# Optimization experiments

Measured on AMD Instinct MI355X. Metric: run time of the kernel, lower is better.

The kernel has to match this reference:

```python
import jax, jax.numpy as jnp
import numpy as np

N_ITERS = 100   # fixed ADMM (OSQP-style) iteration count
RHO = 1.0       # ADMM penalty
SIGMA = 1e-6    # OSQP regularization


def setup_inputs() -> dict:
    key = jax.random.key(0)
    ks = jax.random.split(key, 12)
    B, S, H, nA = 16384, 512, 1024, 24
    mEq, mIneq = 4, 8
    state = jax.random.normal(ks[0], (B, S), dtype=jnp.float32)
    Aeq = jax.random.normal(ks[1], (mEq, nA), dtype=jnp.float32)
    beq = jax.random.normal(ks[2], (mEq,), dtype=jnp.float32)
    A = jax.random.normal(ks[3], (mIneq, nA), dtype=jnp.float32)
    b = jax.random.uniform(ks[4], (mIneq,), dtype=jnp.float32)
    ub = jnp.ones((nA,), dtype=jnp.float32)
    lb = jnp.zeros((nA,), dtype=jnp.float32)
    # MLP parameters (3 Dense layers as in the flax module)
    W1 = jax.random.normal(ks[5], (S, H), dtype=jnp.float32) / np.sqrt(S).astype(np.float32)
    b1 = jnp.zeros((H,), dtype=jnp.float32)
    W2 = jax.random.normal(ks[6], (H, H), dtype=jnp.float32) / np.sqrt(H).astype(np.float32)
    b2 = jnp.zeros((H,), dtype=jnp.float32)
    W3 = jax.random.normal(ks[7], (H, nA), dtype=jnp.float32) / np.sqrt(H).astype(np.float32)
    b3 = jnp.zeros((nA,), dtype=jnp.float32)
    return dict(state=state, Aeq=Aeq, beq=beq, A=A, b=b, ub=ub, lb=lb,
                W1=W1, b1=b1, W2=W2, b2=b2, W3=W3, b3=b3)


def reference(state, Aeq, beq, A, b, ub, lb, W1, b1, W2, b2, W3, b3):
    # ---- 3-layer MLP ----
    h = jax.nn.relu(state @ W1 + b1)
    h = jax.nn.relu(h @ W2 + b2)
    raw = h @ W3 + b3                      # [B, n]
    n = raw.shape[-1]
    I = jnp.eye(n, dtype=raw.dtype)
    # ---- stack constraints exactly as solve_qp: [Aeq; A_ineq; I; -I] ----
    A_tot = jnp.concatenate([Aeq, A, I, -I], axis=0)            # [M, n]
    neg_inf = jnp.full((A.shape[0],), -jnp.inf, dtype=raw.dtype)
    l_tot = jnp.concatenate([beq, neg_inf, lb, -ub])            # [M]
    u_tot = jnp.concatenate([beq, b, ub, -lb])                  # [M]
    # ---- OSQP-style ADMM: min 0.5||x||^2 - raw'x  s.t. l <= A_tot x <= u ----
    q = -raw                                                    # [B, n]
    M = (1.0 + SIGMA) * I + RHO * (A_tot.T @ A_tot)             # [n, n] (P = I)
    Minv = jnp.linalg.inv(M)
    B_, m = q.shape[0], A_tot.shape[0]
    X0 = jnp.zeros_like(q)
    Z0 = jnp.zeros((B_, m), dtype=q.dtype)
    Y0 = jnp.zeros((B_, m), dtype=q.dtype)

    def step(carry, _):
        X, Z, Y = carry
        rhs = SIGMA * X - q + (RHO * Z - Y) @ A_tot             # [B, n]
        Xn = rhs @ Minv.T                                       # [B, n]
        Zt = Xn @ A_tot.T                                       # [B, m]
        Zn = jnp.clip(Zt + Y / RHO, l_tot, u_tot)
        Yn = Y + RHO * (Zt - Zn)
        return (Xn, Zn, Yn), None

    (X, Z, Y), _ = jax.lax.scan(step, (X0, Z0, Y0), None, length=N_ITERS)
    return X
```

## Files before the change

### kernel.cpp

```cpp
#include <hip/hip_runtime.h>

using uint = unsigned int;
using ushort = unsigned short;

typedef __attribute__((ext_vector_type(8))) short bf16x8;
typedef __attribute__((ext_vector_type(4))) short bf16x4;
typedef __attribute__((ext_vector_type(4))) float f32x4;

#define ADMM_ITERS 100
#define RHO_C 1.0f
#define SIGMA_C 1e-6f

__device__ inline ushort f2bf(float f) {
  union { float f; uint u; } c; c.f = f;
  uint u = c.u;
  uint r = (u + 0x7fffu + ((u >> 16) & 1u)) >> 16;
  return (ushort)r;
}

__device__ inline void gload_lds16(const void* g, void* l) {
  __builtin_amdgcn_global_load_lds(
      (const __attribute__((address_space(1))) void*)g,
      (__attribute__((address_space(3))) void*)l, 16, 0, 0);
}

__device__ inline void splitPack(const float* x, bf16x8& hi, bf16x8& lo) {
#pragma unroll
  for (int j = 0; j < 8; ++j) {
    uint b = __float_as_uint(x[j]);
    uint hb = b & 0xffff0000u;
    float lf = x[j] - __uint_as_float(hb);
    hi[j] = (short)(b >> 16);
    lo[j] = (short)(__float_as_uint(lf) >> 16);
  }
}

__device__ inline void packPairs(const f32x4& x, uint& h0, uint& h1,
                                 uint& l0, uint& l1) {
  uint b0 = __float_as_uint(x[0]), b1 = __float_as_uint(x[1]);
  uint b2 = __float_as_uint(x[2]), b3 = __float_as_uint(x[3]);
  float r0 = x[0] - __uint_as_float(b0 & 0xffff0000u);
  float r1 = x[1] - __uint_as_float(b1 & 0xffff0000u);
  float r2 = x[2] - __uint_as_float(b2 & 0xffff0000u);
  float r3 = x[3] - __uint_as_float(b3 & 0xffff0000u);
  h0 = __builtin_amdgcn_perm(b1, b0, 0x07060302u);
  h1 = __builtin_amdgcn_perm(b3, b2, 0x07060302u);
  l0 = __builtin_amdgcn_perm(__float_as_uint(r1), __float_as_uint(r0), 0x07060302u);
  l1 = __builtin_amdgcn_perm(__float_as_uint(r3), __float_as_uint(r2), 0x07060302u);
}

__device__ inline int permrow(int n) {
  if (n < 32) {
    int j = n & 7;
    return ((j >> 2) << 4) + ((n >> 3) << 2) + (j & 3);
  }
  return n;
}

__device__ void transpose_body(const float* __restrict__ in, ushort* __restrict__ out,
                               int R, int C, int Cout, int bx, int by, int tid) {
  __shared__ float t[32][33];
  const int c0 = bx * 32, r0 = by * 32;
  const int tx = tid & 31, ty = tid >> 5;
  for (int rr = ty; rr < 32; rr += 8) {
    int r = r0 + rr, c = c0 + tx;
    float v = 0.0f;
    if (r < R && c < C) v = in[(long)r * C + c];
    t[rr][tx] = v;
  }
  __syncthreads();
  for (int rr = ty; rr < 32; rr += 8) {
    int c = c0 + rr, r = r0 + tx;
    if (c < Cout && r < R) out[(long)c * R + r] = f2bf(t[tx][rr]);
  }
}

__device__ void setup_body(const float* __restrict__ Aeq, const float* __restrict__ beq,
                           const float* __restrict__ A, const float* __restrict__ b,
                           const float* __restrict__ ub, const float* __restrict__ lb,
                           ushort* __restrict__ Th, ushort* __restrict__ Tl,
                           ushort* __restrict__ T0h, ushort* __restrict__ T0l,
                           float* __restrict__ blp, float* __restrict__ bup, int t) {
  __shared__ float Aug[24][48];
  __shared__ float A12[12 * 24];
  __shared__ float fac[24];
  __shared__ float Tx[24][36];
  for (int i = t; i < 48 * 64; i += 256) { Th[i] = 0; Tl[i] = 0; }
  for (int i = t; i < 48 * 32; i += 256) { T0h[i] = 0; T0l[i] = 0; }
  if (t < 96)  A12[t] = Aeq[t];
  if (t < 192) A12[96 + t] = A[t];
  __syncthreads();
  for (int idx = t; idx < 576; idx += 256) {
    int j = idx / 24, k = idx % 24;
    float s = (j == k) ? (1.0f + SIGMA_C + 2.0f * RHO_C) : 0.0f;
    for (int r = 0; r < 12; ++r) s += RHO_C * A12[r * 24 + j] * A12[r * 24 + k];
    Aug[j][k] = s;
    Aug[j][24 + k] = (j == k) ? 1.0f : 0.0f;
  }
  __syncthreads();
  for (int p = 0; p < 24; ++p) {
    float rp = 1.0f / Aug[p][p];
    if (t < 24) fac[t] = Aug[t][p];
    __syncthreads();
    if (t < 48) Aug[p][t] *= rp;
    __syncthreads();
    for (int idx = t; idx < 24 * 48; idx += 256) {
      int r = idx / 48, c = idx % 48;
      if (r != p) Aug[r][c] -= fac[r] * Aug[p][c];
    }
    __syncthreads();
  }
  auto splitStore = [](ushort* hp, ushort* lp, int i, float v) {
    ushort hs = f2bf(v);
    float hf = __uint_as_float(((uint)hs) << 16);
    ushort ls = f2bf(v - hf);
    hp[i] = hs; lp[i] = ls;
  };
  for (int idx = t; idx < 24 * 36; idx += 256) {
    int n = idx / 36, k = idx % 36;
    float v;
    if (k < 24) v = 2.0f * Aug[n][24 + k];
    else {
      v = 0.0f;
      for (int j = 0; j < 24; ++j) v += Aug[n][24 + j] * A12[(k - 24) * 24 + j];
    }
    Tx[n][k] = v;
    splitStore(Th, Tl, permrow(n) * 64 + k, v);
  }
  __syncthreads();
  for (int idx = t; idx < 12 * 36; idx += 256) {
    int m = idx / 36, k = idx % 36;
    float v = 0.0f;
    for (int j = 0; j < 24; ++j) v += A12[m * 24 + j] * Tx[j][k];
    splitStore(Th, Tl, permrow(24 + m) * 64 + k, v);
  }
  for (int idx = t; idx < 36 * 24; idx += 256) {
    int n = idx / 24, k = idx % 24;
    float v;
    if (n < 24) v = Aug[n][24 + k];
    else {
      v = 0.0f;
      for (int j = 0; j < 24; ++j) v += A12[(n - 24) * 24 + j] * Aug[j][24 + k];
    }
    splitStore(T0h, T0l, permrow(n) * 32 + k, v);
  }
  if (t < 48) {
    float lv, uv;
    if (t < 24)      { lv = lb[t]; uv = ub[t]; }
    else if (t < 28) { lv = beq[t - 24]; uv = lv; }
    else if (t < 36) { lv = -1e30f; uv = b[t - 28]; }
    else             { lv = -1e30f; uv = 1e30f; }
    blp[t] = lv; bup[t] = uv;
  }
}

__global__ void prep_all(
    const float* __restrict__ state, ushort* __restrict__ stateB, int n4,
    const float* __restrict__ W1, ushort* __restrict__ W1T,
    const float* __restrict__ W2, ushort* __restrict__ W2T,
    const float* __restrict__ W3, ushort* __restrict__ W3T,
    const float* __restrict__ Aeq, const float* __restrict__ beq,
    const float* __restrict__ A, const float* __restrict__ b,
    const float* __restrict__ ub, const float* __restrict__ lb,
    ushort* __restrict__ Th, ushort* __restrict__ Tl,
    ushort* __restrict__ T0h, ushort* __restrict__ T0l,
    float* __restrict__ blp, float* __restrict__ bup) {
  const int nConv = n4 >> 8;
  int bb = blockIdx.x;
  if (bb < nConv) {
    int i = bb * 256 + threadIdx.x;
    if (i < n4) {
      float4 v = ((const float4*)state)[i];
      uint2 p;
      p.x = (uint)f2bf(v.x) | ((uint)f2bf(v.y) << 16);
      p.y = (uint)f2bf(v.z) | ((uint)f2bf(v.w) << 16);
      ((uint2*)stateB)[i] = p;
    }
    return;
  }
  bb -= nConv;
  if (bb < 512)  { transpose_body(W1, W1T, 512, 1024, 1024, bb & 31, bb >> 5, threadIdx.x); return; }
  bb -= 512;
  if (bb < 1024) { transpose_body(W2, W2T, 1024, 1024, 1024, bb & 31, bb >> 5, threadIdx.x); return; }
  bb -= 1024;
  if (bb < 32)   { transpose_body(W3, W3T, 1024, 24, 32, 0, bb, threadIdx.x); return; }
  setup_body(Aeq, beq, A, b, ub, lb, Th, Tl, T0h, T0l, blp, bup, threadIdx.x);
}

template<int BM, int BN, int WM, int WN, int TM, int TN, int MODE>
__global__ __launch_bounds__(256) void gemm_bt(
    const ushort* __restrict__ A, const ushort* __restrict__ Bt,
    const float* __restrict__ bias, void* __restrict__ Cout_,
    int K, int ldc, int nvalid) {
  __shared__ char lds[(BM + BN) * 64];
  char* ldsA = lds;
  char* ldsB = lds + BM * 64;

  const int tid = threadIdx.x;
  const int wave = tid >> 6;
  const int lane = tid & 63;
  const int blockM = blockIdx.y * BM;
  const int blockN = blockIdx.x * BN;
  const int wm = (wave / WN) * (TM * 16);
  const int wn = (wave % WN) * (TN * 16);

  f32x4 acc[TM][TN] = {};

  const int l15 = lane & 15;
  const int kq = lane >> 4;
  constexpr int AI = BM / 16;
  constexpr int TOT = (BM + BN) / 16;
  const int srow = lane >> 2;
  const int kb = (lane & 3) ^ ((srow >> 1) & 3);

  for (int k0 = 0; k0 < K; k0 += 32) {
    for (int inst = wave; inst < TOT; inst += 4) {
      const bool isA = inst < AI;
      const int i = isA ? inst : inst - AI;
      const ushort* gp = (isA ? A : Bt)
          + (long)((isA ? blockM : blockN) + i * 16 + srow) * K + (k0 + kb * 8);
      char* lp = (isA ? ldsA : ldsB) + i * 1024;
      gload_lds16(gp, lp);
    }
    __syncthreads();

    bf16x8 af[TM], bfr[TN];
#pragma unroll
    for (int i = 0; i < TM; ++i) {
      int r = wm + i * 16 + l15;
      int ch = kq ^ ((r >> 1) & 3);
      af[i] = *(const bf16x8*)(ldsA + r * 64 + ch * 16);
    }
#pragma unroll
    for (int j = 0; j < TN; ++j) {
      int r = wn + j * 16 + l15;
      int ch = kq ^ ((r >> 1) & 3);
      bfr[j] = *(const bf16x8*)(ldsB + r * 64 + ch * 16);
    }
#pragma unroll
    for (int i = 0; i < TM; ++i)
#pragma unroll
      for (int j = 0; j < TN; ++j)
        acc[i][j] = __builtin_amdgcn_mfma_f32_16x16x32_bf16(af[i], bfr[j], acc[i][j], 0, 0, 0);
    __syncthreads();
  }

  const int ro = lane >> 4;
#pragma unroll
  for (int i = 0; i < TM; ++i) {
#pragma unroll
    for (int j = 0; j < TN; ++j) {
      const int col = blockN + wn + j * 16 + l15;
      float bv;
      if (MODE == 0) bv = bias[col];
      else bv = (col < nvalid) ? bias[col] : 0.0f;
#pragma unroll
      for (int r = 0; r < 4; ++r) {
        const int row = blockM + wm + i * 16 + ro * 4 + r;
        float v = acc[i][j][r] + bv;
        if (MODE == 0) {
          v = fmaxf(v, 0.0f);
          ((ushort*)Cout_)[(long)row * ldc + col] = f2bf(v);
        } else {
          if (col < nvalid) ((float*)Cout_)[(long)row * ldc + col] = v;
        }
      }
    }
  }
}

#define GEMM8P_QUAD(MI0, NJ0)                                                 \
  _Pragma("unroll") for (int mi_ = 0; mi_ < 4; ++mi_)                         \
  _Pragma("unroll") for (int nj_ = 0; nj_ < 2; ++nj_)                         \
  _Pragma("unroll") for (int kk_ = 0; kk_ < 2; ++kk_)                         \
    acc[(MI0) + mi_][(NJ0) + nj_] = __builtin_amdgcn_mfma_f32_16x16x32_bf16(  \
        aF[mi_][kk_], bF[(NJ0) + nj_][kk_], acc[(MI0) + mi_][(NJ0) + nj_],    \
        0, 0, 0);

#define GEMM8P_SYNC_PRE()                              \
  __builtin_amdgcn_s_barrier();                        \
  asm volatile("s_waitcnt lgkmcnt(0)" ::: "memory");   \
  __builtin_amdgcn_sched_barrier(0);                   \
  __builtin_amdgcn_s_setprio(1);

#define GEMM8P_SYNC_POST()                             \
  __builtin_amdgcn_s_setprio(0);                       \
  __builtin_amdgcn_s_barrier();

__global__ __launch_bounds__(512, 2) void gemm8p(
    const ushort* __restrict__ A, const ushort* __restrict__ Bt,
    const float* __restrict__ bias, ushort* __restrict__ Cout,
    int K, int ldc, int nblk_n) {
  __shared__ __align__(16) char ldsc[131072];

  const int nwg = gridDim.x;
  const int bid = blockIdx.x;
  const int swz = (bid & 7) * (nwg >> 3) + (bid >> 3);
  const int blockM = (swz / nblk_n) * 256;
  const int blockN = (swz % nblk_n) * 256;

  const int tid = threadIdx.x;
  const int wave = tid >> 6;
  const int lane = tid & 63;
  const int l15 = lane & 15;
  const int q = lane >> 4;
  const int wm = (wave >> 2) * 128;
  const int wn = (wave & 3) * 64;
  const int nt = K >> 6;

  f32x4 acc[8][4] = {};

  auto stage = [&](int ts, int h) {
    if (ts >= nt) return;
    char* base = ldsc + ((ts & 1) << 16) + (h << 14);
#pragma unroll
    for (int j = 0; j < 2; ++j) {
      const int idx = wave * 64 + j * 512 + lane;
      const int row = idx >> 3;
      const int cs = (idx & 7) ^ (row & 7);
      const ushort* gp =
          (h < 2 ? A + (long)(blockM + ((h & 1) << 7) + row) * K
                 : Bt + (long)(blockN + ((h & 1) << 7) + row) * K)
          + (ts << 6) + cs * 8;
      gload_lds16(gp, base + ((wave * 64 + j * 512) << 4));
    }
  };
  auto dsA = [&](int cb, int mi, int kk) {
    const int r = wm + mi * 16 + l15;
    const int cs = (kk * 4 + q) ^ (r & 7);
    return *(const bf16x8*)(ldsc + (cb << 16) + r * 128 + cs * 16);
  };
  auto dsB = [&](int cb, int nj, int kk) {
    const int r = wn + nj * 16 + l15;
    const int cs = (kk * 4 + q) ^ (r & 7);
    return *(const bf16x8*)(ldsc + (cb << 16) + 32768 + r * 128 + cs * 16);
  };

  stage(0, 0); stage(0, 1); stage(0, 2); stage(0, 3);
  stage(1, 0);
  asm volatile("s_waitcnt vmcnt(2)" ::: "memory");
  __builtin_amdgcn_s_barrier();

  bf16x8 aF[4][2], bF[4][2];
#pragma unroll 1
  for (int t = 0; t < nt; ++t) {
    const int cb = t & 1;
#pragma unroll
    for (int mi = 0; mi < 4; ++mi)
#pragma unroll
      for (int kk = 0; kk < 2; ++kk) aF[mi][kk] = dsA(cb, mi, kk);
#pragma unroll
    for (int nj = 0; nj < 2; ++nj)
#pragma unroll
      for (int kk = 0; kk < 2; ++kk) bF[nj][kk] = dsB(cb, nj, kk);
    stage(t + 1, 1);
    GEMM8P_SYNC_PRE();
    GEMM8P_QUAD(0, 0);
    GEMM8P_SYNC_POST();
#pragma unroll
    for (int nj = 2; nj < 4; ++nj)
#pragma unroll
      for (int kk = 0; kk < 2; ++kk) bF[nj][kk] = dsB(cb, nj, kk);
    stage(t + 1, 2);
    GEMM8P_SYNC_PRE();
    GEMM8P_QUAD(0, 2);
    GEMM8P_SYNC_POST();
#pragma unroll
    for (int mi = 0; mi < 4; ++mi)
#pragma unroll
      for (int kk = 0; kk < 2; ++kk) aF[mi][kk] = dsA(cb, 4 + mi, kk);
    stage(t + 1, 3);
    GEMM8P_SYNC_PRE();
    GEMM8P_QUAD(4, 2);
    GEMM8P_SYNC_POST();
    stage(t + 2, 0);
    if (t + 2 < nt) { asm volatile("s_waitcnt vmcnt(2)" ::: "memory"); }
    else            { asm volatile("s_waitcnt vmcnt(0)" ::: "memory"); }
    __builtin_amdgcn_s_barrier();
    __builtin_amdgcn_s_setprio(1);
    GEMM8P_QUAD(4, 0);
    GEMM8P_SYNC_POST();
  }

#pragma unroll
  for (int mi = 0; mi < 8; ++mi) {
#pragma unroll
    for (int nj = 0; nj < 4; ++nj) {
      const int col = blockN + wn + nj * 16 + l15;
      const float bv = bias[col];
#pragma unroll
      for (int r = 0; r < 4; ++r) {
        const int row = blockM + wm + mi * 16 + q * 4 + r;
        float v = acc[mi][nj][r] + bv;
        v = fmaxf(v, 0.0f);
        Cout[(long)row * ldc + col] = f2bf(v);
      }
    }
  }
}

__global__ __launch_bounds__(64) void admm_mfma(
    const float* __restrict__ raw,
    const ushort* __restrict__ Th, const ushort* __restrict__ Tl,
    const ushort* __restrict__ T0h, const ushort* __restrict__ T0l,
    const float* __restrict__ blp, const float* __restrict__ bup,
    float* __restrict__ outp) {
  const int lane = threadIdx.x & 63;
  const int l15 = lane & 15, q = lane >> 4;
  const long rowbase = (long)blockIdx.x * 16;

  f32x4 bl[3], bu[3];
  bl[0] = *(const f32x4*)(blp + 8 * q);
  bu[0] = *(const f32x4*)(bup + 8 * q);
  bl[1] = *(const f32x4*)(blp + 8 * q + 4);
  bu[1] = *(const f32x4*)(bup + 8 * q + 4);
  bl[2] = *(const f32x4*)(blp + 32 + 4 * q);
  bu[2] = *(const f32x4*)(bup + 32 + 4 * q);

  f32x4 W[3], base[3];
  {
    bf16x8 t0h[3], t0l[3];
#pragma unroll
    for (int t = 0; t < 3; ++t) {
      t0h[t] = *(const bf16x8*)(T0h + (16 * t + l15) * 32 + q * 8);
      t0l[t] = *(const bf16x8*)(T0l + (16 * t + l15) * 32 + q * 8);
    }
    float qa[8];
    if (q < 3) {
      const float* rp = raw + (rowbase + l15) * 24 + q * 8;
      float4 v0 = *(const float4*)rp;
      float4 v1 = *(const float4*)(rp + 4);
      qa[0] = v0.x; qa[1] = v0.y; qa[2] = v0.z; qa[3] = v0.w;
      qa[4] = v1.x; qa[5] = v1.y; qa[6] = v1.z; qa[7] = v1.w;
    } else {
#pragma unroll
      for (int j = 0; j < 8; ++j) qa[j] = 0.0f;
    }
    bf16x8 qhi, qlo;
    splitPack(qa, qhi, qlo);
#pragma unroll
    for (int t = 0; t < 3; ++t) {
      f32x4 acc = {0.0f, 0.0f, 0.0f, 0.0f};
      acc = __builtin_amdgcn_mfma_f32_16x16x32_bf16(t0h[t], qhi, acc, 0, 0, 0);
      acc = __builtin_amdgcn_mfma_f32_16x16x32_bf16(t0h[t], qlo, acc, 0, 0, 0);
      acc = __builtin_amdgcn_mfma_f32_16x16x32_bf16(t0l[t], qhi, acc, 0, 0, 0);
      base[t] = acc; W[t] = acc;
    }
  }

  bf16x8 th[3][2], tl[3][2];
#pragma unroll
  for (int t = 0; t < 3; ++t)
#pragma unroll
    for (int c = 0; c < 2; ++c) {
      th[t][c] = *(const bf16x8*)(Th + (16 * t + l15) * 64 + 32 * c + q * 8);
      tl[t][c] = *(const bf16x8*)(Tl + (16 * t + l15) * 64 + 32 * c + q * 8);
    }

#define CLIPU(t, U_, CC)                                             \
  _Pragma("unroll") for (int r = 0; r < 4; ++r) {                    \
    float w_ = W[t][r];                                              \
    float z_ = fminf(fmaxf(w_, bl[t][r]), bu[t][r]);                 \
    float yy_ = w_ - z_;                                             \
    U_[r] = z_ - yy_;                                                \
    CC[r] = base[t][r] + yy_;                                        \
  }

#pragma unroll 1
  for (int it = 2; it < ADMM_ITERS; ++it) {
    f32x4 u0, u1, u2, C0, C1, C2;
    CLIPU(0, u0, C0);
    CLIPU(1, u1, C1);
    CLIPU(2, u2, C2);
    union { uint d[4]; bf16x8 v; } uh0, ul0, uh1, ul1;
    packPairs(u0, uh0.d[0], uh0.d[1], ul0.d[0], ul0.d[1]);
    packPairs(u1, uh0.d[2], uh0.d[3], ul0.d[2], ul0.d[3]);
    packPairs(u2, uh1.d[0], uh1.d[1], ul1.d[0], ul1.d[1]);
    uh1.d[2] = 0; uh1.d[3] = 0; ul1.d[2] = 0; ul1.d[3] = 0;
    f32x4 a0 = C0, a1 = C1, a2 = C2;
    a0 = __builtin_amdgcn_mfma_f32_16x16x32_bf16(th[0][0], uh0.v, a0, 0, 0, 0);
    a1 = __builtin_amdgcn_mfma_f32_16x16x32_bf16(th[1][0], uh0.v, a1, 0, 0, 0);
    a2 = __builtin_amdgcn_mfma_f32_16x16x32_bf16(th[2][0], uh0.v, a2, 0, 0, 0);
    a0 = __builtin_amdgcn_mfma_f32_16x16x32_bf16(th[0][1], uh1.v, a0, 0, 0, 0);
    a1 = __builtin_amdgcn_mfma_f32_16x16x32_bf16(th[1][1], uh1.v, a1, 0, 0, 0);
    a2 = __builtin_amdgcn_mfma_f32_16x16x32_bf16(th[2][1], uh1.v, a2, 0, 0, 0);
    a0 = __builtin_amdgcn_mfma_f32_16x16x32_bf16(th[0][0], ul0.v, a0, 0, 0, 0);
    a1 = __builtin_amdgcn_mfma_f32_16x16x32_bf16(th[1][0], ul0.v, a1, 0, 0, 0);
    a2 = __builtin_amdgcn_mfma_f32_16x16x32_bf16(th[2][0], ul0.v, a2, 0, 0, 0);
    a0 = __builtin_amdgcn_mfma_f32_16x16x32_bf16(th[0][1], ul1.v, a0, 0, 0, 0);
    a1 = __builtin_amdgcn_mfma_f32_16x16x32_bf16(th[1][1], ul1.v, a1, 0, 0, 0);
    a2 = __builtin_amdgcn_mfma_f32_16x16x32_bf16(th[2][1], ul1.v, a2, 0, 0, 0);
    a0 = __builtin_amdgcn_mfma_f32_16x16x32_bf16(tl[0][0], uh0.v, a0, 0, 0, 0);
    a1 = __builtin_amdgcn_mfma_f32_16x16x32_bf16(tl[1][0], uh0.v, a1, 0, 0, 0);
    a2 = __builtin_amdgcn_mfma_f32_16x16x32_bf16(tl[2][0], uh0.v, a2, 0, 0, 0);
    a0 = __builtin_amdgcn_mfma_f32_16x16x32_bf16(tl[0][1], uh1.v, a0, 0, 0, 0);
    a1 = __builtin_amdgcn_mfma_f32_16x16x32_bf16(tl[1][1], uh1.v, a1, 0, 0, 0);
    a2 = __builtin_amdgcn_mfma_f32_16x16x32_bf16(tl[2][1], uh1.v, a2, 0, 0, 0);
    W[0] = a0; W[1] = a1; W[2] = a2;
  }

  {
    f32x4 u0, u1, u2, C0, C1, C2;
    CLIPU(0, u0, C0);
    CLIPU(1, u1, C1);
    CLIPU(2, u2, C2);
    union { uint d[4]; bf16x8 v; } uh0, ul0, uh1, ul1;
    packPairs(u0, uh0.d[0], uh0.d[1], ul0.d[0], ul0.d[1]);
    packPairs(u1, uh0.d[2], uh0.d[3], ul0.d[2], ul0.d[3]);
    packPairs(u2, uh1.d[0], uh1.d[1], ul1.d[0], ul1.d[1]);
    uh1.d[2] = 0; uh1.d[3] = 0; ul1.d[2] = 0; ul1.d[3] = 0;
    f32x4 x0 = base[0], x1 = base[1];
    x0 = __builtin_amdgcn_mfma_f32_16x16x32_bf16(th[0][0], uh0.v, x0, 0, 0, 0);
    x1 = __builtin_amdgcn_mfma_f32_16x16x32_bf16(th[1][0], uh0.v, x1, 0, 0, 0);
    x0 = __builtin_amdgcn_mfma_f32_16x16x32_bf16(th[0][1], uh1.v, x0, 0, 0, 0);
    x1 = __builtin_amdgcn_mfma_f32_16x16x32_bf16(th[1][1], uh1.v, x1, 0, 0, 0);
    x0 = __builtin_amdgcn_mfma_f32_16x16x32_bf16(th[0][0], ul0.v, x0, 0, 0, 0);
    x1 = __builtin_amdgcn_mfma_f32_16x16x32_bf16(th[1][0], ul0.v, x1, 0, 0, 0);
    x0 = __builtin_amdgcn_mfma_f32_16x16x32_bf16(th[0][1], ul1.v, x0, 0, 0, 0);
    x1 = __builtin_amdgcn_mfma_f32_16x16x32_bf16(th[1][1], ul1.v, x1, 0, 0, 0);
    x0 = __builtin_amdgcn_mfma_f32_16x16x32_bf16(tl[0][0], uh0.v, x0, 0, 0, 0);
    x1 = __builtin_amdgcn_mfma_f32_16x16x32_bf16(tl[1][0], uh0.v, x1, 0, 0, 0);
    x0 = __builtin_amdgcn_mfma_f32_16x16x32_bf16(tl[0][1], uh1.v, x0, 0, 0, 0);
    x1 = __builtin_amdgcn_mfma_f32_16x16x32_bf16(tl[1][1], uh1.v, x1, 0, 0, 0);
    if (q < 3) {
      float* op = outp + (rowbase + l15) * 24 + 8 * q;
      *(f32x4*)op = x0;
      *(f32x4*)(op + 4) = x1;
    }
  }
#undef CLIPU
}

extern "C" void kernel_launch(void* const* d_in, const int* in_sizes, int n_in,
                              void* d_out, int out_size, void* d_ws, size_t ws_size,
                              hipStream_t stream) {
  const float* state = (const float*)d_in[0];
  const float* Aeq   = (const float*)d_in[1];
  const float* beq   = (const float*)d_in[2];
  const float* Ain   = (const float*)d_in[3];
  const float* bin   = (const float*)d_in[4];
  const float* ub    = (const float*)d_in[5];
  const float* lb    = (const float*)d_in[6];
  const float* W1    = (const float*)d_in[7];
  const float* b1    = (const float*)d_in[8];
  const float* W2    = (const float*)d_in[9];
  const float* b2    = (const float*)d_in[10];
  const float* W3    = (const float*)d_in[11];
  const float* b3    = (const float*)d_in[12];

  const int Bn = in_sizes[0] / 512;
  char* ws = (char*)d_ws;
  ushort* stateB = (ushort*)(ws + 0);
  ushort* W1T    = (ushort*)(ws + 16777216);
  ushort* W2T    = (ushort*)(ws + 17825792);
  ushort* W3T    = (ushort*)(ws + 19922944);
  ushort* Th     = (ushort*)(ws + 19993600);
  ushort* Tl     = (ushort*)(ws + 19999744);
  ushort* T0h    = (ushort*)(ws + 20005888);
  ushort* T0l    = (ushort*)(ws + 20008960);
  float*  blp    = (float*) (ws + 20012032);
  float*  bup    = (float*) (ws + 20012224);
  ushort* H1     = (ushort*)(ws + 21565440);
  ushort* H2     = (ushort*)(ws + 55119872);
  float*  rawb   = (float*)d_out;

  const int n4 = (Bn * 512) / 4;
  const int nConv = n4 / 256;
  const int nPrep = nConv + 512 + 1024 + 32 + 1;
  prep_all<<<nPrep, 256, 0, stream>>>(state, stateB, n4, W1, W1T, W2, W2T, W3, W3T,
                                      Aeq, beq, Ain, bin, ub, lb,
                                      Th, Tl, T0h, T0l, blp, bup);

  const int nblkN = 1024 / 256;
  const int nwg = (Bn / 256) * nblkN;
  gemm8p<<<nwg, 512, 0, stream>>>(stateB, W1T, b1, H1, 512, 1024, nblkN);
  gemm8p<<<nwg, 512, 0, stream>>>(H1, W2T, b2, H2, 1024, 1024, nblkN);
  gemm_bt<64, 32, 4, 1, 1, 2, 1><<<dim3(1, Bn / 64), 256, 0, stream>>>(
      H2, W3T, b3, rawb, 1024, 24, 24);

  admm_mfma<<<Bn / 16, 64, 0, stream>>>(rawb, Th, Tl, T0h, T0l, blp, bup,
                                        (float*)d_out);
}
```

Baseline: 267.6 us.

## Interleave two independent row groups per wave in ADMM kernel

Each ADMM wave now processes two 16-row groups and software-pipelines them, so the clip/pack VALU work of one group is issued alongside the MFMA chain of the other. This is meant to hide the serial dependency latency between the MFMA results and the next iteration's clip. The trade-offs are more registers per wave and half as many workgroups (Bn/32 instead of Bn/16). The iteration count is preserved: one VALU step before the loop, 97 loop iterations and one peeled MFMA step per group, then the epilogue.

```diff
diff --git a/kernel.cpp b/kernel.cpp
--- a/kernel.cpp
+++ b/kernel.cpp
@@ -399,6 +399,77 @@
   }
 }
 
+#define MF(a, b, c) __builtin_amdgcn_mfma_f32_16x16x32_bf16(a, b, c, 0, 0, 0)
+
+#define CLIP4(Wv, basev, t, Uv, Cv)                                  \
+  _Pragma("unroll") for (int r = 0; r < 4; ++r) {                    \
+    float w_ = Wv[t][r];                                             \
+    float z_ = fminf(fmaxf(w_, bl[t][r]), bu[t][r]);                 \
+    float yy_ = w_ - z_;                                             \
+    Uv[r] = z_ - yy_;                                                \
+    Cv[r] = basev[t][r] + yy_;                                       \
+  }
+
+#define VALU_GRP(Wv, basev, UH0, UL0, UH1, UL1, C0, C1, C2)          \
+  {                                                                  \
+    f32x4 u0_, u1_, u2_;                                             \
+    CLIP4(Wv, basev, 0, u0_, C0);                                    \
+    CLIP4(Wv, basev, 1, u1_, C1);                                    \
+    CLIP4(Wv, basev, 2, u2_, C2);                                    \
+    union { uint d[4]; bf16x8 v; } h0_, l0_, h1_, l1_;               \
+    packPairs(u0_, h0_.d[0], h0_.d[1], l0_.d[0], l0_.d[1]);          \
+    packPairs(u1_, h0_.d[2], h0_.d[3], l0_.d[2], l0_.d[3]);          \
+    packPairs(u2_, h1_.d[0], h1_.d[1], l1_.d[0], l1_.d[1]);          \
+    h1_.d[2] = 0; h1_.d[3] = 0; l1_.d[2] = 0; l1_.d[3] = 0;          \
+    UH0 = h0_.v; UL0 = l0_.v; UH1 = h1_.v; UL1 = l1_.v;              \
+  }
+
+#define MFMA_GRP(Wv, UH0, UL0, UH1, UL1, C0, C1, C2)                 \
+  {                                                                  \
+    f32x4 a0_ = C0, a1_ = C1, a2_ = C2;                              \
+    a0_ = MF(th[0][0], UH0, a0_);                                    \
+    a1_ = MF(th[1][0], UH0, a1_);                                    \
+    a2_ = MF(th[2][0], UH0, a2_);                                    \
+    a0_ = MF(th[0][1], UH1, a0_);                                    \
+    a1_ = MF(th[1][1], UH1, a1_);                                    \
+    a2_ = MF(th[2][1], UH1, a2_);                                    \
+    a0_ = MF(th[0][0], UL0, a0_);                                    \
+    a1_ = MF(th[1][0], UL0, a1_);                                    \
+    a2_ = MF(th[2][0], UL0, a2_);                                    \
+    a0_ = MF(th[0][1], UL1, a0_);                                    \
+    a1_ = MF(th[1][1], UL1, a1_);                                    \
+    a2_ = MF(th[2][1], UL1, a2_);                                    \
+    a0_ = MF(tl[0][0], UH0, a0_);                                    \
+    a1_ = MF(tl[1][0], UH0, a1_);                                    \
+    a2_ = MF(tl[2][0], UH0, a2_);                                    \
+    a0_ = MF(tl[0][1], UH1, a0_);                                    \
+    a1_ = MF(tl[1][1], UH1, a1_);                                    \
+    a2_ = MF(tl[2][1], UH1, a2_);                                    \
+    Wv[0] = a0_; Wv[1] = a1_; Wv[2] = a2_;                           \
+  }
+
+#define EPI_GRP(basev, UH0, UL0, UH1, UL1, rb)                       \
+  {                                                                  \
+    f32x4 x0_ = basev[0], x1_ = basev[1];                            \
+    x0_ = MF(th[0][0], UH0, x0_);                                    \
+    x1_ = MF(th[1][0], UH0, x1_);                                    \
+    x0_ = MF(th[0][1], UH1, x0_);                                    \
+    x1_ = MF(th[1][1], UH1, x1_);                                    \
+    x0_ = MF(th[0][0], UL0, x0_);                                    \
+    x1_ = MF(th[1][0], UL0, x1_);                                    \
+    x0_ = MF(th[0][1], UL1, x0_);                                    \
+    x1_ = MF(th[1][1], UL1, x1_);                                    \
+    x0_ = MF(tl[0][0], UH0, x0_);                                    \
+    x1_ = MF(tl[1][0], UH0, x1_);                                    \
+    x0_ = MF(tl[0][1], UH1, x0_);                                    \
+    x1_ = MF(tl[1][1], UH1, x1_);                                    \
+    if (q < 3) {                                                     \
+      float* op_ = outp + ((rb) + l15) * 24 + 8 * q;                 \
+      *(f32x4*)op_ = x0_;                                            \
+      *(f32x4*)(op_ + 4) = x1_;                                      \
+    }                                                                \
+  }
+
 __global__ __launch_bounds__(64) void admm_mfma(
     const float* __restrict__ raw,
     const ushort* __restrict__ Th, const ushort* __restrict__ Tl,
@@ -407,7 +478,8 @@
     float* __restrict__ outp) {
   const int lane = threadIdx.x & 63;
   const int l15 = lane & 15, q = lane >> 4;
-  const long rowbase = (long)blockIdx.x * 16;
+  const long rowG = (long)blockIdx.x * 32;
+  const long rowH = rowG + 16;
 
   f32x4 bl[3], bu[3];
   bl[0] = *(const f32x4*)(blp + 8 * q);
@@ -417,7 +489,7 @@
   bl[2] = *(const f32x4*)(blp + 32 + 4 * q);
   bu[2] = *(const f32x4*)(bup + 32 + 4 * q);
 
-  f32x4 W[3], base[3];
+  f32x4 WG[3], baseG[3], WH[3], baseH[3];
   {
     bf16x8 t0h[3], t0l[3];
 #pragma unroll
@@ -425,26 +497,31 @@
       t0h[t] = *(const bf16x8*)(T0h + (16 * t + l15) * 32 + q * 8);
       t0l[t] = *(const bf16x8*)(T0l + (16 * t + l15) * 32 + q * 8);
     }
-    float qa[8];
-    if (q < 3) {
-      const float* rp = raw + (rowbase + l15) * 24 + q * 8;
-      float4 v0 = *(const float4*)rp;
-      float4 v1 = *(const float4*)(rp + 4);
-      qa[0] = v0.x; qa[1] = v0.y; qa[2] = v0.z; qa[3] = v0.w;
-      qa[4] = v1.x; qa[5] = v1.y; qa[6] = v1.z; qa[7] = v1.w;
-    } else {
-#pragma unroll
-      for (int j = 0; j < 8; ++j) qa[j] = 0.0f;
-    }
-    bf16x8 qhi, qlo;
-    splitPack(qa, qhi, qlo);
-#pragma unroll
-    for (int t = 0; t < 3; ++t) {
-      f32x4 acc = {0.0f, 0.0f, 0.0f, 0.0f};
-      acc = __builtin_amdgcn_mfma_f32_16x16x32_bf16(t0h[t], qhi, acc, 0, 0, 0);
-      acc = __builtin_amdgcn_mfma_f32_16x16x32_bf16(t0h[t], qlo, acc, 0, 0, 0);
-      acc = __builtin_amdgcn_mfma_f32_16x16x32_bf16(t0l[t], qhi, acc, 0, 0, 0);
-      base[t] = acc; W[t] = acc;
+#pragma unroll
+    for (int g = 0; g < 2; ++g) {
+      const long rb = g ? rowH : rowG;
+      float qa[8];
+      if (q < 3) {
+        const float* rp = raw + (rb + l15) * 24 + q * 8;
+        float4 v0 = *(const float4*)rp;
+        float4 v1 = *(const float4*)(rp + 4);
+        qa[0] = v0.x; qa[1] = v0.y; qa[2] = v0.z; qa[3] = v0.w;
+        qa[4] = v1.x; qa[5] = v1.y; qa[6] = v1.z; qa[7] = v1.w;
+      } else {
+#pragma unroll
+        for (int j = 0; j < 8; ++j) qa[j] = 0.0f;
+      }
+      bf16x8 qhi, qlo;
+      splitPack(qa, qhi, qlo);
+#pragma unroll
+      for (int t = 0; t < 3; ++t) {
+        f32x4 acc = {0.0f, 0.0f, 0.0f, 0.0f};
+        acc = MF(t0h[t], qhi, acc);
+        acc = MF(t0h[t], qlo, acc);
+        acc = MF(t0l[t], qhi, acc);
+        if (g) { baseH[t] = acc; WH[t] = acc; }
+        else   { baseG[t] = acc; WG[t] = acc; }
+      }
     }
   }
 
@@ -457,78 +534,26 @@
       tl[t][c] = *(const bf16x8*)(Tl + (16 * t + l15) * 64 + 32 * c + q * 8);
     }
 
-#define CLIPU(t, U_, CC)                                             \
-  _Pragma("unroll") for (int r = 0; r < 4; ++r) {                    \
-    float w_ = W[t][r];                                              \
-    float z_ = fminf(fmaxf(w_, bl[t][r]), bu[t][r]);                 \
-    float yy_ = w_ - z_;                                             \
-    U_[r] = z_ - yy_;                                                \
-    CC[r] = base[t][r] + yy_;                                        \
-  }
+  bf16x8 gH0, gL0, gH1, gL1, hH0, hL0, hH1, hL1;
+  f32x4 gC0, gC1, gC2, hC0, hC1, hC2;
+
+  VALU_GRP(WG, baseG, gH0, gL0, gH1, gL1, gC0, gC1, gC2);
 
 #pragma unroll 1
-  for (int it = 2; it < ADMM_ITERS; ++it) {
-    f32x4 u0, u1, u2, C0, C1, C2;
-    CLIPU(0, u0, C0);
-    CLIPU(1, u1, C1);
-    CLIPU(2, u2, C2);
-    union { uint d[4]; bf16x8 v; } uh0, ul0, uh1, ul1;
-    packPairs(u0, uh0.d[0], uh0.d[1], ul0.d[0], ul0.d[1]);
-    packPairs(u1, uh0.d[2], uh0.d[3], ul0.d[2], ul0.d[3]);
-    packPairs(u2, uh1.d[0], uh1.d[1], ul1.d[0], ul1.d[1]);
-    uh1.d[2] = 0; uh1.d[3] = 0; ul1.d[2] = 0; ul1.d[3] = 0;
-    f32x4 a0 = C0, a1 = C1, a2 = C2;
-    a0 = __builtin_amdgcn_mfma_f32_16x16x32_bf16(th[0][0], uh0.v, a0, 0, 0, 0);
-    a1 = __builtin_amdgcn_mfma_f32_16x16x32_bf16(th[1][0], uh0.v, a1, 0, 0, 0);
-    a2 = __builtin_amdgcn_mfma_f32_16x16x32_bf16(th[2][0], uh0.v, a2, 0, 0, 0);
-    a0 = __builtin_amdgcn_mfma_f32_16x16x32_bf16(th[0][1], uh1.v, a0, 0, 0, 0);
-    a1 = __builtin_amdgcn_mfma_f32_16x16x32_bf16(th[1][1], uh1.v, a1, 0, 0, 0);
-    a2 = __builtin_amdgcn_mfma_f32_16x16x32_bf16(th[2][1], uh1.v, a2, 0, 0, 0);
-    a0 = __builtin_amdgcn_mfma_f32_16x16x32_bf16(th[0][0], ul0.v, a0, 0, 0, 0);
-    a1 = __builtin_amdgcn_mfma_f32_16x16x32_bf16(th[1][0], ul0.v, a1, 0, 0, 0);
-    a2 = __builtin_amdgcn_mfma_f32_16x16x32_bf16(th[2][0], ul0.v, a2, 0, 0, 0);
-    a0 = __builtin_amdgcn_mfma_f32_16x16x32_bf16(th[0][1], ul1.v, a0, 0, 0, 0);
-    a1 = __builtin_amdgcn_mfma_f32_16x16x32_bf16(th[1][1], ul1.v, a1, 0, 0, 0);
-    a2 = __builtin_amdgcn_mfma_f32_16x16x32_bf16(th[2][1], ul1.v, a2, 0, 0, 0);
-    a0 = __builtin_amdgcn_mfma_f32_16x16x32_bf16(tl[0][0], uh0.v, a0, 0, 0, 0);
-    a1 = __builtin_amdgcn_mfma_f32_16x16x32_bf16(tl[1][0], uh0.v, a1, 0, 0, 0);
-    a2 = __builtin_amdgcn_mfma_f32_16x16x32_bf16(tl[2][0], uh0.v, a2, 0, 0, 0);
-    a0 = __builtin_amdgcn_mfma_f32_16x16x32_bf16(tl[0][1], uh1.v, a0, 0, 0, 0);
-    a1 = __builtin_amdgcn_mfma_f32_16x16x32_bf16(tl[1][1], uh1.v, a1, 0, 0, 0);
-    a2 = __builtin_amdgcn_mfma_f32_16x16x32_bf16(tl[2][1], uh1.v, a2, 0, 0, 0);
-    W[0] = a0; W[1] = a1; W[2] = a2;
-  }
-
-  {
-    f32x4 u0, u1, u2, C0, C1, C2;
-    CLIPU(0, u0, C0);
-    CLIPU(1, u1, C1);
-    CLIPU(2, u2, C2);
-    union { uint d[4]; bf16x8 v; } uh0, ul0, uh1, ul1;
-    packPairs(u0, uh0.d[0], uh0.d[1], ul0.d[0], ul0.d[1]);
-    packPairs(u1, uh0.d[2], uh0.d[3], ul0.d[2], ul0.d[3]);
-    packPairs(u2, uh1.d[0], uh1.d[1], ul1.d[0], ul1.d[1]);
-    uh1.d[2] = 0; uh1.d[3] = 0; ul1.d[2] = 0; ul1.d[3] = 0;
-    f32x4 x0 = base[0], x1 = base[1];
-    x0 = __builtin_amdgcn_mfma_f32_16x16x32_bf16(th[0][0], uh0.v, x0, 0, 0, 0);
-    x1 = __builtin_amdgcn_mfma_f32_16x16x32_bf16(th[1][0], uh0.v, x1, 0, 0, 0);
-    x0 = __builtin_amdgcn_mfma_f32_16x16x32_bf16(th[0][1], uh1.v, x0, 0, 0, 0);
-    x1 = __builtin_amdgcn_mfma_f32_16x16x32_bf16(th[1][1], uh1.v, x1, 0, 0, 0);
-    x0 = __builtin_amdgcn_mfma_f32_16x16x32_bf16(th[0][0], ul0.v, x0, 0, 0, 0);
-    x1 = __builtin_amdgcn_mfma_f32_16x16x32_bf16(th[1][0], ul0.v, x1, 0, 0, 0);
-    x0 = __builtin_amdgcn_mfma_f32_16x16x32_bf16(th[0][1], ul1.v, x0, 0, 0, 0);
-    x1 = __builtin_amdgcn_mfma_f32_16x16x32_bf16(th[1][1], ul1.v, x1, 0, 0, 0);
-    x0 = __builtin_amdgcn_mfma_f32_16x16x32_bf16(tl[0][0], uh0.v, x0, 0, 0, 0);
-    x1 = __builtin_amdgcn_mfma_f32_16x16x32_bf16(tl[1][0], uh0.v, x1, 0, 0, 0);
-    x0 = __builtin_amdgcn_mfma_f32_16x16x32_bf16(tl[0][1], uh1.v, x0, 0, 0, 0);
-    x1 = __builtin_amdgcn_mfma_f32_16x16x32_bf16(tl[1][1], uh1.v, x1, 0, 0, 0);
-    if (q < 3) {
-      float* op = outp + (rowbase + l15) * 24 + 8 * q;
-      *(f32x4*)op = x0;
-      *(f32x4*)(op + 4) = x1;
-    }
-  }
-#undef CLIPU
+  for (int it = 2; it < ADMM_ITERS - 1; ++it) {
+    MFMA_GRP(WG, gH0, gL0, gH1, gL1, gC0, gC1, gC2);
+    VALU_GRP(WH, baseH, hH0, hL0, hH1, hL1, hC0, hC1, hC2);
+    MFMA_GRP(WH, hH0, hL0, hH1, hL1, hC0, hC1, hC2);
+    VALU_GRP(WG, baseG, gH0, gL0, gH1, gL1, gC0, gC1, gC2);
+  }
+  MFMA_GRP(WG, gH0, gL0, gH1, gL1, gC0, gC1, gC2);
+  VALU_GRP(WH, baseH, hH0, hL0, hH1, hL1, hC0, hC1, hC2);
+  MFMA_GRP(WH, hH0, hL0, hH1, hL1, hC0, hC1, hC2);
+
+  VALU_GRP(WG, baseG, gH0, gL0, gH1, gL1, gC0, gC1, gC2);
+  VALU_GRP(WH, baseH, hH0, hL0, hH1, hL1, hC0, hC1, hC2);
+  EPI_GRP(baseG, gH0, gL0, gH1, gL1, rowG);
+  EPI_GRP(baseH, hH0, hL0, hH1, hL1, rowH);
 }
 
 extern "C" void kernel_launch(void* const* d_in, const int* in_sizes, int n_in,
@@ -578,6 +603,6 @@
   gemm_bt<64, 32, 4, 1, 1, 2, 1><<<dim3(1, Bn / 64), 256, 0, stream>>>(
       H2, W3T, b3, rawb, 1024, 24, 24);
 
-  admm_mfma<<<Bn / 16, 64, 0, stream>>>(rawb, Th, Tl, T0h, T0l, blp, bup,
+  admm_mfma<<<Bn / 32, 64, 0, stream>>>(rawb, Th, Tl, T0h, T0l, blp, bup,
                                         (float*)d_out);
 }
```

After: 263.6 us. About the same (-1.5%).
